# Optimization experiments

Measured on AMD Instinct MI355X. Metric: run time of the kernel, lower is better.

Reference implementation:

```python
import jax, jax.numpy as jnp
import numpy as np

B, S, H = 8, 256, 128
LA, LR = 2, 2
L = LA + LR
HD = H // L  # head_size = 32
SCALE = 1.0 / np.sqrt(HD).astype(np.float32)


def setup_inputs() -> dict:
    key = jax.random.key(0)
    ks = jax.random.split(key, 16)
    w = 0.02
    return {
        'hidden_states': jax.random.normal(ks[0], (B, S, H), jnp.float32),
        'attention_mask': jnp.zeros((B, 1, S, S), jnp.float32),
        'abs0': jax.random.normal(ks[1], (B, S, H), jnp.float32),
        'abs1': jax.random.normal(ks[2], (B, S, H), jnp.float32),
        'rel0': jax.random.normal(ks[3], (B, S, S, H), jnp.float32),
        'rel1': jax.random.normal(ks[4], (B, S, S, H), jnp.float32),
        'Wq': jax.random.normal(ks[5], (H, H), jnp.float32) * w,
        'bq': jnp.zeros((H,), jnp.float32),
        'Wk': jax.random.normal(ks[6], (H, H), jnp.float32) * w,
        'bk': jnp.zeros((H,), jnp.float32),
        'Wv': jax.random.normal(ks[7], (H, H), jnp.float32) * w,
        'bv': jnp.zeros((H,), jnp.float32),
        'Wo': jax.random.normal(ks[8], (H, H), jnp.float32) * w,
        'bo': jnp.zeros((H,), jnp.float32),
    }


def reference(hidden_states, attention_mask, abs0, abs1, rel0, rel1,
              Wq, bq, Wk, bk, Wv, bv, Wo, bo):
    # Projections; heads dim is L (= La+Lr), head size HD
    Q = (hidden_states @ Wq + bq).reshape(B, S, L, HD).transpose(0, 2, 1, 3)  # [B,L,S,HD]
    K = (hidden_states @ Wk + bk).reshape(B, S, L, HD).transpose(0, 2, 1, 3)
    V = (hidden_states @ Wv + bv).reshape(B, S, L, HD).transpose(0, 2, 1, 3)

    scores = jnp.einsum('blqh,blkh->blqk', Q, K) * SCALE  # [B,L,S,S]

    # Absolute-kernel heads 0..La-1: key-project only head i's slice of Wk
    for i, ae in enumerate((abs0, abs1)):
        aK = ae @ Wk[:, i * HD:(i + 1) * HD] + bk[i * HD:(i + 1) * HD]  # [B,S,HD]
        scores = scores.at[:, i].add(jnp.einsum('bqh,bkh->bqk', Q[:, i], aK) * SCALE)

    # Relative-kernel heads La..L-1: per-(q,k) relative key slice
    for i, re in enumerate((rel0, rel1)):
        h = LA + i
        rK = re @ Wk[:, h * HD:(h + 1) * HD] + bk[h * HD:(h + 1) * HD]  # [B,S,S,HD]
        scores = scores.at[:, h].add(jnp.einsum('bqh,bqkh->bqk', Q[:, h], rK) * SCALE)

    scores = scores + attention_mask
    probs = jax.nn.softmax(scores, axis=-1)  # [B,L,S,S]

    ctx = jnp.einsum('blqk,blkh->blqh', probs, V)  # [B,L,S,HD]

    for i, ae in enumerate((abs0, abs1)):
        aV = ae @ Wv[:, i * HD:(i + 1) * HD] + bv[i * HD:(i + 1) * HD]  # [B,S,HD]
        ctx = ctx.at[:, i].add(jnp.einsum('bqk,bkh->bqh', probs[:, i], aV))

    for i, re in enumerate((rel0, rel1)):
        h = LA + i
        rV = re @ Wv[:, h * HD:(h + 1) * HD] + bv[h * HD:(h + 1) * HD]  # [B,S,S,HD]
        ctx = ctx.at[:, h].add(jnp.einsum('bqk,bqkh->bqh', probs[:, h], rV))

    ctx = ctx.transpose(0, 2, 1, 3).reshape(B, S, H)
    return ctx @ Wo + bo
```

## Files before the change

### kernel.cpp

```cpp
#include <hip/hip_runtime.h>

#define Bc 8
#define Sc 256
#define Hc 128
#define HDc 32
#define NHc 4
#define SCALE 0.17677669529663687f

__global__ __launch_bounds__(256, 4) void mmha_kernel(
    const float* __restrict__ hs,
    const float* __restrict__ am,
    const float* __restrict__ abs0,
    const float* __restrict__ abs1,
    const float* __restrict__ rel0,
    const float* __restrict__ rel1,
    const float* __restrict__ Wq, const float* __restrict__ bq,
    const float* __restrict__ Wk, const float* __restrict__ bk,
    const float* __restrict__ Wv, const float* __restrict__ bv,
    const float* __restrict__ Wo, const float* __restrict__ bo,
    float* __restrict__ out)
{
    const int t = threadIdx.x;
    const int bqi = blockIdx.x;
    const int b = bqi >> 8;
    const int q = bqi & 255;

    __shared__ float hsrow[Hc];
    __shared__ float Qrow[Hc];
    __shared__ float qk_sh[NHc * Hc];
    __shared__ float cb_sh[NHc];
    __shared__ float mask_row[Sc];
    __shared__ float4 red4[256];
    __shared__ float l_sh[8];
    __shared__ float rbarn[NHc * 132];
    __shared__ float ctx_sh[Hc];

    const size_t rowbase = (size_t)(b * Sc + q) * Hc;

    if (t < Hc) hsrow[t] = hs[rowbase + t];
    mask_row[t] = am[((size_t)(b * Sc) + q) * Sc + t];
    __syncthreads();

    if (t < Hc) {
        float acc = bq[t];
        #pragma unroll 16
        for (int c = 0; c < Hc; ++c) acc += hsrow[c] * Wq[c * Hc + t];
        Qrow[t] = acc;
    }
    __syncthreads();

    if (t < Hc) {
        float pv = Qrow[t] * bk[t];
        #pragma unroll
        for (int off = 16; off >= 1; off >>= 1) pv += __shfl_xor(pv, off, 32);
        if ((t & 31) == 0) cb_sh[t >> 5] = 2.0f * pv;
    }
    for (int rep = 0; rep < 2; ++rep) {
        int idx = rep * 256 + t;
        int h = idx >> 7, cp = idx & 127;
        const float4* wkr = (const float4*)(Wk + cp * Hc + h * HDc);
        const float4* qr  = (const float4*)(Qrow + h * HDc);
        float acc = 0.f;
        #pragma unroll
        for (int j = 0; j < HDc / 4; ++j) {
            float4 wv = wkr[j];
            float4 qv = qr[j];
            acc += wv.x * qv.x + wv.y * qv.y + wv.z * qv.z + wv.w * qv.w;
        }
        qk_sh[h * Hc + cp] = acc;
    }
    __syncthreads();

    const int c4 = t & 31;
    const int part = t >> 5;

    const float4* hs4 = (const float4*)(hs)   + (size_t)b * Sc * (Hc / 4);
    const float4* e0p = (const float4*)(abs0) + (size_t)b * Sc * (Hc / 4);
    const float4* e1p = (const float4*)(abs1) + (size_t)b * Sc * (Hc / 4);
    const float4* e2p = (const float4*)(rel0) + (size_t)(b * Sc + q) * Sc * (Hc / 4);
    const float4* e3p = (const float4*)(rel1) + (size_t)(b * Sc + q) * Sc * (Hc / 4);

    float4 qreg[NHc];
    float  cbr[NHc];
    float4 acc[NHc];
    float  l[NHc];
    #pragma unroll
    for (int h = 0; h < NHc; ++h) {
        qreg[h] = ((const float4*)(qk_sh + h * Hc))[c4];
        cbr[h]  = cb_sh[h];
        acc[h].x = acc[h].y = acc[h].z = acc[h].w = 0.f;
        l[h] = 0.f;
    }

    #pragma unroll 2
    for (int r = 0; r < 32; ++r) {
        const int row = r * 8 + part;
        const int off = row * (Hc / 4) + c4;
        const float4 a = hs4[off];
        float4 e[NHc];
        e[0] = e0p[off];
        e[1] = e1p[off];
        e[2] = e2p[off];
        e[3] = e3p[off];
        const float m = mask_row[row];
        #pragma unroll
        for (int h = 0; h < NHc; ++h) {
            float4 v;
            v.x = a.x + e[h].x; v.y = a.y + e[h].y;
            v.z = a.z + e[h].z; v.w = a.w + e[h].w;
            float pv = v.x * qreg[h].x + v.y * qreg[h].y
                     + v.z * qreg[h].z + v.w * qreg[h].w;
            #pragma unroll
            for (int o = 16; o >= 1; o >>= 1) pv += __shfl_xor(pv, o, 32);
            const float p = __expf((pv + cbr[h]) * SCALE + m);
            l[h] += p;
            acc[h].x += p * v.x; acc[h].y += p * v.y;
            acc[h].z += p * v.z; acc[h].w += p * v.w;
        }
    }

    #pragma unroll
    for (int h = 0; h < NHc; ++h) {
        __syncthreads();
        red4[t] = acc[h];
        if (c4 == 0) l_sh[part] = l[h];
        __syncthreads();
        if (t < 32) {
            float4 tot; tot.x = tot.y = tot.z = tot.w = 0.f;
            #pragma unroll
            for (int g = 0; g < 8; ++g) {
                float4 v = red4[g * 32 + t];
                tot.x += v.x; tot.y += v.y; tot.z += v.z; tot.w += v.w;
            }
            float lt = 0.f;
            #pragma unroll
            for (int g = 0; g < 8; ++g) lt += l_sh[g];
            const float inv = 1.0f / lt;
            float4 rv; rv.x = tot.x * inv; rv.y = tot.y * inv;
                       rv.z = tot.z * inv; rv.w = tot.w * inv;
            ((float4*)(rbarn + h * 132))[t] = rv;
        }
    }
    __syncthreads();

    if (t < Hc) {
        const float* rb = rbarn + (t >> 5) * 132;
        float cv = 2.0f * bv[t];
        #pragma unroll 8
        for (int c = 0; c < Hc; ++c) cv += rb[c] * Wv[c * Hc + t];
        ctx_sh[t] = cv;
    }
    __syncthreads();

    if (t < Hc) {
        float ov = bo[t];
        #pragma unroll 16
        for (int c = 0; c < Hc; ++c) ov += ctx_sh[c] * Wo[c * Hc + t];
        out[rowbase + t] = ov;
    }
}

extern "C" void kernel_launch(void* const* d_in, const int* in_sizes, int n_in,
                              void* d_out, int out_size, void* d_ws, size_t ws_size,
                              hipStream_t stream) {
    const float* hs = (const float*)d_in[0];
    const float* am = (const float*)d_in[1];
    const float* a0 = (const float*)d_in[2];
    const float* a1 = (const float*)d_in[3];
    const float* r0 = (const float*)d_in[4];
    const float* r1 = (const float*)d_in[5];
    const float* Wq = (const float*)d_in[6];
    const float* bq = (const float*)d_in[7];
    const float* Wk = (const float*)d_in[8];
    const float* bk = (const float*)d_in[9];
    const float* Wv = (const float*)d_in[10];
    const float* bv = (const float*)d_in[11];
    const float* Wo = (const float*)d_in[12];
    const float* bo = (const float*)d_in[13];

    mmha_kernel<<<dim3(Bc * Sc), dim3(256), 0, stream>>>(
        hs, am, a0, a1, r0, r1, Wq, bq, Wk, bk, Wv, bv, Wo, bo, (float*)d_out);
}
```

Measured before the change: 596.7 us.

## Software-prefetch streamed rows, DPP warp reductions, and single-pass cross-head reduction

The main loop now keeps a register ring of upcoming rows. The hs/abs rows are prefetched two iterations ahead and the rel rows four ahead, so the global-memory latency of the large rel tensor streams overlaps with compute. The 32-lane dot-product reduction uses DPP row shifts plus one shuffle instead of five shuffles. The per-head block reductions are merged into one shared-memory pass, which needs fewer barriers. In exchange the kernel uses more registers and a larger aliased shared buffer, which may cut occupancy under the launch bound of 4 blocks.

```diff
diff --git a/kernel.cpp b/kernel.cpp
--- a/kernel.cpp
+++ b/kernel.cpp
@@ -6,6 +6,19 @@
 #define HDc 32
 #define NHc 4
 #define SCALE 0.17677669529663687f
+
+__device__ __forceinline__ float red32(float x) {
+    x += __int_as_float(__builtin_amdgcn_update_dpp(
+            0, __float_as_int(x), 0x121, 0xF, 0xF, false));
+    x += __int_as_float(__builtin_amdgcn_update_dpp(
+            0, __float_as_int(x), 0x122, 0xF, 0xF, false));
+    x += __int_as_float(__builtin_amdgcn_update_dpp(
+            0, __float_as_int(x), 0x124, 0xF, 0xF, false));
+    x += __int_as_float(__builtin_amdgcn_update_dpp(
+            0, __float_as_int(x), 0x128, 0xF, 0xF, false));
+    x += __shfl_xor(x, 16, 32);
+    return x;
+}
 
 __global__ __launch_bounds__(256, 4) void mmha_kernel(
     const float* __restrict__ hs,
@@ -25,15 +38,13 @@
     const int b = bqi >> 8;
     const int q = bqi & 255;
 
-    __shared__ float hsrow[Hc];
-    __shared__ float Qrow[Hc];
-    __shared__ float qk_sh[NHc * Hc];
-    __shared__ float cb_sh[NHc];
-    __shared__ float mask_row[Sc];
-    __shared__ float4 red4[256];
-    __shared__ float l_sh[8];
-    __shared__ float rbarn[NHc * 132];
-    __shared__ float ctx_sh[Hc];
+    __shared__ float4 smem4[1196];
+    float* sm = (float*)smem4;
+    float* hsrow    = sm;
+    float* Qrow     = sm + 128;
+    float* qk_sh    = sm + 256;
+    float* cb_sh    = sm + 768;
+    float* mask_row = sm + 772;
 
     const size_t rowbase = (size_t)(b * Sc + q) * Hc;
 
@@ -73,6 +84,7 @@
 
     const int c4 = t & 31;
     const int part = t >> 5;
+    const int boff = part * 32 + c4;
 
     const float4* hs4 = (const float4*)(hs)   + (size_t)b * Sc * (Hc / 4);
     const float4* e0p = (const float4*)(abs0) + (size_t)b * Sc * (Hc / 4);
@@ -81,81 +93,116 @@
     const float4* e3p = (const float4*)(rel1) + (size_t)(b * Sc + q) * Sc * (Hc / 4);
 
     float4 qreg[NHc];
-    float  cbr[NHc];
+    float  cbs[NHc];
     float4 acc[NHc];
     float  l[NHc];
     #pragma unroll
     for (int h = 0; h < NHc; ++h) {
         qreg[h] = ((const float4*)(qk_sh + h * Hc))[c4];
-        cbr[h]  = cb_sh[h];
+        cbs[h]  = cb_sh[h] * SCALE;
         acc[h].x = acc[h].y = acc[h].z = acc[h].w = 0.f;
         l[h] = 0.f;
     }
 
-    #pragma unroll 2
-    for (int r = 0; r < 32; ++r) {
-        const int row = r * 8 + part;
-        const int off = row * (Hc / 4) + c4;
-        const float4 a = hs4[off];
-        float4 e[NHc];
-        e[0] = e0p[off];
-        e[1] = e1p[off];
-        e[2] = e2p[off];
-        e[3] = e3p[off];
-        const float m = mask_row[row];
-        #pragma unroll
-        for (int h = 0; h < NHc; ++h) {
-            float4 v;
-            v.x = a.x + e[h].x; v.y = a.y + e[h].y;
-            v.z = a.z + e[h].z; v.w = a.w + e[h].w;
-            float pv = v.x * qreg[h].x + v.y * qreg[h].y
-                     + v.z * qreg[h].z + v.w * qreg[h].w;
-            #pragma unroll
-            for (int o = 16; o >= 1; o >>= 1) pv += __shfl_xor(pv, o, 32);
-            const float p = __expf((pv + cbr[h]) * SCALE + m);
-            l[h] += p;
-            acc[h].x += p * v.x; acc[h].y += p * v.y;
-            acc[h].z += p * v.z; acc[h].w += p * v.w;
+    float4 A[2], E0[2], E1[2], E2[4], E3[4];
+    A[0]  = hs4[boff];        A[1]  = hs4[boff + 256];
+    E0[0] = e0p[boff];        E0[1] = e0p[boff + 256];
+    E1[0] = e1p[boff];        E1[1] = e1p[boff + 256];
+    E2[0] = e2p[boff];        E2[1] = e2p[boff + 256];
+    E2[2] = e2p[boff + 512];  E2[3] = e2p[boff + 768];
+    E3[0] = e3p[boff];        E3[1] = e3p[boff + 256];
+    E3[2] = e3p[boff + 512];  E3[3] = e3p[boff + 768];
+
+#define HEAD(i, f)                                                          \
+    {                                                                       \
+        float4 v;                                                           \
+        v.x = a.x + (f).x; v.y = a.y + (f).y;                               \
+        v.z = a.z + (f).z; v.w = a.w + (f).w;                               \
+        float pv = red32(v.x * qreg[i].x + v.y * qreg[i].y                  \
+                       + v.z * qreg[i].z + v.w * qreg[i].w);                \
+        const float p = __expf(pv * SCALE + (cbs[i] + ml));                 \
+        l[i] += p;                                                          \
+        acc[i].x += p * v.x; acc[i].y += p * v.y;                           \
+        acc[i].z += p * v.z; acc[i].w += p * v.w;                           \
+    }
+
+#define STEP(K)                                                             \
+    do {                                                                    \
+        const float4 a  = A[(K) & 1];                                       \
+        const float4 f0 = E0[(K) & 1];                                      \
+        const float4 f1 = E1[(K) & 1];                                      \
+        const float4 f2 = E2[(K) & 3];                                      \
+        const float4 f3 = E3[(K) & 3];                                      \
+        const float ml = mask_row[(r + (K)) * 8 + part];                    \
+        {                             \
+            int rn = r + (K) + 2; if (rn > 31) rn = 31;                     \
+            const int offn = rn * 256 + boff;                               \
+            A[(K) & 1]  = hs4[offn];                                        \
+            E0[(K) & 1] = e0p[offn];                                        \
+            E1[(K) & 1] = e1p[offn];                                        \
+        }                                                                   \
+        {                        \
+            int rn = r + (K) + 4; if (rn > 31) rn = 31;                     \
+            const int offn = rn * 256 + boff;                               \
+            E2[(K) & 3] = e2p[offn];                                        \
+            E3[(K) & 3] = e3p[offn];                                        \
+        }                                                                   \
+        HEAD(0, f0)                                                         \
+        HEAD(1, f1)                                                         \
+        HEAD(2, f2)                                                         \
+        HEAD(3, f3)                                                         \
+    } while (0)
+
+    for (int r = 0; r < 32; r += 4) {
+        STEP(0);
+        STEP(1);
+        STEP(2);
+        STEP(3);
+    }
+#undef STEP
+#undef HEAD
+
+    __syncthreads();
+    float4* redA = (float4*)sm;
+    #pragma unroll
+    for (int h = 0; h < NHc; ++h) redA[h * 256 + t] = acc[h];
+    if (c4 == 0) {
+        #pragma unroll
+        for (int h = 0; h < NHc; ++h) sm[4096 + h * 8 + part] = l[h];
+    }
+    __syncthreads();
+    if (t < 128) {
+        const int h = t >> 5, j = t & 31;
+        float4 tot; tot.x = tot.y = tot.z = tot.w = 0.f;
+        #pragma unroll
+        for (int g = 0; g < 8; ++g) {
+            float4 vv = redA[h * 256 + g * 32 + j];
+            tot.x += vv.x; tot.y += vv.y; tot.z += vv.z; tot.w += vv.w;
         }
-    }
-
-    #pragma unroll
-    for (int h = 0; h < NHc; ++h) {
-        __syncthreads();
-        red4[t] = acc[h];
-        if (c4 == 0) l_sh[part] = l[h];
-        __syncthreads();
-        if (t < 32) {
-            float4 tot; tot.x = tot.y = tot.z = tot.w = 0.f;
-            #pragma unroll
-            for (int g = 0; g < 8; ++g) {
-                float4 v = red4[g * 32 + t];
-                tot.x += v.x; tot.y += v.y; tot.z += v.z; tot.w += v.w;
-            }
-            float lt = 0.f;
-            #pragma unroll
-            for (int g = 0; g < 8; ++g) lt += l_sh[g];
-            const float inv = 1.0f / lt;
-            float4 rv; rv.x = tot.x * inv; rv.y = tot.y * inv;
-                       rv.z = tot.z * inv; rv.w = tot.w * inv;
-            ((float4*)(rbarn + h * 132))[t] = rv;
-        }
-    }
-    __syncthreads();
-
-    if (t < Hc) {
-        const float* rb = rbarn + (t >> 5) * 132;
+        float lt = 0.f;
+        #pragma unroll
+        for (int g = 0; g < 8; ++g) lt += sm[4096 + h * 8 + g];
+        const float inv = 1.0f / lt;
+        float4 rv; rv.x = tot.x * inv; rv.y = tot.y * inv;
+                   rv.z = tot.z * inv; rv.w = tot.w * inv;
+        ((float4*)(sm + 4128 + h * 132))[j] = rv;
+    }
+    __syncthreads();
+
+    if (t < Hc) {
+        const float* rb = sm + 4128 + (t >> 5) * 132;
         float cv = 2.0f * bv[t];
         #pragma unroll 8
         for (int c = 0; c < Hc; ++c) cv += rb[c] * Wv[c * Hc + t];
-        ctx_sh[t] = cv;
+        sm[4656 + t] = cv;
     }
     __syncthreads();
 
     if (t < Hc) {
         float ov = bo[t];
+        const float* cx = sm + 4656;
         #pragma unroll 16
-        for (int c = 0; c < Hc; ++c) ov += ctx_sh[c] * Wo[c * Hc + t];
+        for (int c = 0; c < Hc; ++c) ov += cx[c] * Wo[c * Hc + t];
         out[rowbase + t] = ov;
     }
 }
```

Result: no change. 585.5 us (-1.9%).
